# Kernel tuning notes

Hardware: AMD Instinct MI355X
Metric: run time of the kernel (lower is better)

Reference implementation:

```python
import jax, jax.numpy as jnp
import numpy as np

N_NODES = 50000
N_EDGES = 800000
OUT_DIM = 394
BN_EPS = 1e-5


def setup_inputs() -> dict:
    key = jax.random.key(0)
    ks = jax.random.split(key, 10)
    x = jax.random.normal(ks[0], (N_NODES, 2), dtype=jnp.float32)
    edge_index = jax.random.randint(ks[1], (2, N_EDGES), 0, N_NODES, dtype=jnp.int64)
    W_gcn = jax.random.normal(ks[2], (OUT_DIM, 2), dtype=jnp.float32) * 0.5
    b_gcn = jax.random.normal(ks[3], (OUT_DIM,), dtype=jnp.float32) * 0.1
    bn_gamma = jax.random.normal(ks[4], (OUT_DIM,), dtype=jnp.float32) * 0.1 + 1.0
    bn_beta = jax.random.normal(ks[5], (OUT_DIM,), dtype=jnp.float32) * 0.1
    bn_mean = jax.random.normal(ks[6], (OUT_DIM,), dtype=jnp.float32) * 0.1
    bn_var = jax.random.uniform(ks[7], (OUT_DIM,), dtype=jnp.float32, minval=0.5, maxval=1.5)
    fc_w = jax.random.normal(ks[8], (OUT_DIM, OUT_DIM), dtype=jnp.float32) * (1.0 / np.sqrt(OUT_DIM))
    fc_b = jax.random.normal(ks[9], (OUT_DIM,), dtype=jnp.float32) * 0.1
    return {"x": x, "edge_index": edge_index, "W_gcn": W_gcn, "b_gcn": b_gcn,
            "bn_gamma": bn_gamma, "bn_beta": bn_beta, "bn_mean": bn_mean,
            "bn_var": bn_var, "fc_w": fc_w, "fc_b": fc_b}


def reference(x, edge_index, W_gcn, b_gcn, bn_gamma, bn_beta, bn_mean, bn_var, fc_w, fc_b):
    n = x.shape[0]
    loop = jnp.arange(n, dtype=edge_index.dtype)
    # PyG GCNConv: add self-loops, symmetric deg^{-1/2} normalization
    src = jnp.concatenate([edge_index[0], loop])  # [E+N] message sources
    dst = jnp.concatenate([edge_index[1], loop])  # [E+N] message targets
    deg = jax.ops.segment_sum(jnp.ones_like(dst, dtype=x.dtype), dst, num_segments=n)
    dinv = jnp.where(deg > 0, jax.lax.rsqrt(deg), 0.0)
    norm = dinv[src] * dinv[dst]  # [E+N]
    xl = x @ W_gcn.T  # [N, 394] linear transform before aggregation
    msgs = xl[src] * norm[:, None]  # [E+N, 394] gathered + normalized messages
    agg = jax.ops.segment_sum(msgs, dst, num_segments=n) + b_gcn  # scatter-add
    h = jax.nn.relu(agg)
    # BatchNorm1d in eval mode (running stats)
    h = (h - bn_mean) * jax.lax.rsqrt(bn_var + BN_EPS) * bn_gamma + bn_beta
    # dropout is a no-op in eval mode
    z = h @ fc_w.T + fc_b
    return (jax.nn.log_softmax(z, axis=1), z)
```

## Files before the change

kernel.cpp:

```cpp
#include <hip/hip_runtime.h>
#include <math.h>

#define DIM 394
#define KP  416
#define NT  13
#define NP  448
#define BN_EPS 1e-5f
#define MAXD 32
#define TST 452

typedef __bf16 bf16x8 __attribute__((ext_vector_type(8)));
typedef float  f32x4  __attribute__((ext_vector_type(4)));

__device__ inline bool edges_are_int32(const int* ei) {
    int l = threadIdx.x & 63;
    unsigned long long b = __ballot(ei[2 * l + 1] != 0);
    return b != 0ULL;
}


__global__ void prep_kernel(const float* __restrict__ Wg, const float* __restrict__ bg,
                            const float* __restrict__ gamma, const float* __restrict__ beta,
                            const float* __restrict__ mean, const float* __restrict__ var,
                            const float* __restrict__ fcw,
                            uint4* __restrict__ zbase, float4* __restrict__ Pk,
                            float* __restrict__ Ok, bf16x8* __restrict__ Bp,
                            int z4, int zb) {
    int b = blockIdx.x, t = threadIdx.x;
    if (b < zb) {
        int i = b * 256 + t;
        if (i < z4) zbase[i] = make_uint4(0u, 0u, 0u, 0u);
    } else if (b < zb + 2) {
        int k = (b - zb) * 256 + t;
        if (k < KP) {
            float4 p = make_float4(0.f, 0.f, 0.f, 0.f);
            float o = 0.f;
            if (k < DIM) {
                p.x = Wg[2 * k];
                p.y = Wg[2 * k + 1];
                p.z = bg[k];
                float sc = gamma[k] * rsqrtf(var[k] + BN_EPS);
                p.w = sc;
                o = beta[k] - sc * mean[k];
            }
            Pk[k] = p;
            Ok[k] = o;
        }
    } else {
        int idx = (b - zb - 2) * 256 + t;
        if (idx < NT * 4 * NP) {
            int col = idx % NP;
            int r   = idx / NP;
            int k0  = r * 8;
            bf16x8 v;
            #pragma unroll
            for (int q = 0; q < 8; ++q) {
                int k = k0 + q;
                float f = (col < DIM && k < DIM) ? fcw[col * DIM + k] : 0.0f;
                v[q] = (__bf16)f;
            }
            Bp[idx] = v;
        }
    }
}

__global__ void place_kernel(const int* __restrict__ ei,
                             unsigned* __restrict__ degc,
                             unsigned* __restrict__ payload,
                             unsigned* __restrict__ ocnt,
                             uint2* __restrict__ olist, int e) {
    bool is32 = edges_are_int32(ei);
    int i0 = (blockIdx.x * blockDim.x + threadIdx.x) * 4;
    if (i0 >= e) return;
    int s[4], d[4];
    int cnt = 4;
    if (i0 + 4 <= e) {
        if (is32) {
            int4 sv = *reinterpret_cast<const int4*>(&ei[i0]);
            int4 dv = *reinterpret_cast<const int4*>(&ei[e + i0]);
            s[0] = sv.x; s[1] = sv.y; s[2] = sv.z; s[3] = sv.w;
            d[0] = dv.x; d[1] = dv.y; d[2] = dv.z; d[3] = dv.w;
        } else {
            int4 a = *reinterpret_cast<const int4*>(&ei[2 * i0]);
            int4 bb = *reinterpret_cast<const int4*>(&ei[2 * i0 + 4]);
            int4 c = *reinterpret_cast<const int4*>(&ei[2 * (e + i0)]);
            int4 dd = *reinterpret_cast<const int4*>(&ei[2 * (e + i0) + 4]);
            s[0] = a.x; s[1] = a.z; s[2] = bb.x; s[3] = bb.z;
            d[0] = c.x; d[1] = c.z; d[2] = dd.x; d[3] = dd.z;
        }
    } else {
        cnt = e - i0;
        for (int j = 0; j < cnt; ++j) {
            s[j] = is32 ? ei[i0 + j]     : ei[2 * (i0 + j)];
            d[j] = is32 ? ei[e + i0 + j] : ei[2 * (e + i0 + j)];
        }
    }
    #pragma unroll
    for (int j = 0; j < 4; ++j) {
        if (j >= cnt) break;
        unsigned tk = atomicAdd(&degc[d[j]], 1u);
        if (tk < MAXD) {
            payload[(size_t)d[j] * MAXD + tk] = (unsigned)s[j];
        } else {
            unsigned o = atomicAdd(ocnt, 1u);
            olist[o] = make_uint2((unsigned)s[j], (unsigned)d[j]);
        }
    }
}

__global__ void cleanup_kernel(const uint2* __restrict__ olist,
                               const unsigned* __restrict__ ocnt,
                               const unsigned* __restrict__ degc,
                               const float2* __restrict__ x2,
                               float* __restrict__ yover) {
    unsigned cnt = *ocnt;
    int gstride = gridDim.x * blockDim.x;
    for (unsigned i = blockIdx.x * blockDim.x + threadIdx.x; i < cnt; i += gstride) {
        uint2 sd = olist[i];
        float ds = rsqrtf(1.0f + (float)degc[sd.x]);
        float2 xv = x2[sd.x];
        atomicAdd(&yover[2 * sd.y],     ds * xv.x);
        atomicAdd(&yover[2 * sd.y + 1], ds * xv.y);
    }
}

__global__ __launch_bounds__(256, 2)
void gemm_fused(const float2* __restrict__ x2, const unsigned* __restrict__ degc,
                const unsigned* __restrict__ payload, const float* __restrict__ yover,
                const float4* __restrict__ Pk, const float* __restrict__ Ok,
                const bf16x8* __restrict__ Bp, const float* __restrict__ fcb,
                float* __restrict__ outp, float* __restrict__ z, int n) {
    __shared__ alignas(16) char smem[16 * TST * 4 + 64];
    bf16x8* As   = (bf16x8*)smem;
    float2* red  = (float2*)(smem + 8192);
    float*  T    = (float*)smem;
    float*  lsebuf = (float*)(smem + 16 * TST * 4);

    int tid = threadIdx.x;
    int wv  = tid >> 6;
    int l   = tid & 63;
    int cg_ = tid & 15;
    int kg  = l >> 4;
    int row0 = blockIdx.x * 64;
    int gi = row0 + l;

    float y0 = 0.f, y1 = 0.f;
    {
        float2 psum = make_float2(0.f, 0.f);
        float dinv_i = 0.f;
        float2 xi = make_float2(0.f, 0.f);
        if (gi < n) {
            unsigned dg = degc[gi];
            dinv_i = rsqrtf(1.0f + (float)dg);
            xi = x2[gi];
            unsigned m = dg < MAXD ? dg : MAXD;
            const unsigned* pl = payload + (size_t)gi * MAXD;
            for (unsigned t = wv; t < m; t += 4) {
                unsigned s = pl[t];
                float2 xv = x2[s];
                float ds = rsqrtf(1.0f + (float)degc[s]);
                psum.x = fmaf(ds, xv.x, psum.x);
                psum.y = fmaf(ds, xv.y, psum.y);
            }
            if (wv == 0) {
                psum.x += yover[2 * gi];
                psum.y += yover[2 * gi + 1];
            }
        }
        red[l * 4 + wv] = psum;
        __syncthreads();
        if (gi < n) {
            float sx = red[l * 4 + 0].x + red[l * 4 + 1].x + red[l * 4 + 2].x + red[l * 4 + 3].x;
            float sy = red[l * 4 + 0].y + red[l * 4 + 1].y + red[l * 4 + 2].y + red[l * 4 + 3].y;
            y0 = dinv_i * (sx + dinv_i * xi.x);
            y1 = dinv_i * (sy + dinv_i * xi.y);
        }
        __syncthreads();
    }

    f32x4 acc[4][7];
    #pragma unroll
    for (int a = 0; a < 4; ++a)
        #pragma unroll
        for (int b = 0; b < 7; ++b)
            acc[a][b] = (f32x4){0.f, 0.f, 0.f, 0.f};

    auto stageA = [&](int ks, int buf) {
        int kb = ks * 32 + wv * 8;
        bf16x8 hv;
        #pragma unroll
        for (int q = 0; q < 8; ++q) {
            float4 p = Pk[kb + q];
            float t = fmaf(y0, p.x, fmaf(y1, p.y, p.z));
            t = fmaxf(t, 0.f);
            hv[q] = (__bf16)fmaf(p.w, t, Ok[kb + q]);
        }
        As[buf * 256 + wv * 64 + l] = hv;
    };

    const bf16x8* bptr = Bp + (kg * 448 + wv * 112 + cg_);

    bf16x8 Bcur[7], Bnxt[7];
    #pragma unroll
    for (int c = 0; c < 7; ++c) Bcur[c] = bptr[c * 16];
    stageA(0, 0);
    __syncthreads();

    int buf = 0;
    for (int ks = 0; ks < NT; ++ks) {
        if (ks < NT - 1) {
            const bf16x8* bn = bptr + (size_t)(ks + 1) * (4 * 448);
            #pragma unroll
            for (int c = 0; c < 7; ++c) Bnxt[c] = bn[c * 16];
            stageA(ks + 1, buf ^ 1);
        }
        bf16x8 af[4];
        #pragma unroll
        for (int rt = 0; rt < 4; ++rt)
            af[rt] = As[buf * 256 + kg * 64 + rt * 16 + cg_];
        #pragma unroll
        for (int ct = 0; ct < 7; ++ct)
            #pragma unroll
            for (int rt = 0; rt < 4; ++rt)
                acc[rt][ct] = __builtin_amdgcn_mfma_f32_16x16x32_bf16(
                                  af[rt], Bcur[ct], acc[rt][ct], 0, 0, 0);
        __syncthreads();
        #pragma unroll
        for (int c = 0; c < 7; ++c) Bcur[c] = Bnxt[c];
        buf ^= 1;
    }

    float* redm = (float*)smem;
    float* reds = redm + 256;

    int colb = wv * 112;
    float bias[7];
    bool  cv[7];
    #pragma unroll
    for (int ct = 0; ct < 7; ++ct) {
        int c = colb + ct * 16 + cg_;
        cv[ct] = (c < DIM);
        bias[ct] = cv[ct] ? fcb[c] : 0.f;
    }
    #pragma unroll
    for (int rt = 0; rt < 4; ++rt)
        #pragma unroll
        for (int ct = 0; ct < 7; ++ct)
            acc[rt][ct] = acc[rt][ct] + bias[ct];

    f32x4 mx[4];
    #pragma unroll
    for (int rt = 0; rt < 4; ++rt) {
        f32x4 m = (f32x4){-1e30f, -1e30f, -1e30f, -1e30f};
        #pragma unroll
        for (int ct = 0; ct < 7; ++ct) {
            if (!cv[ct]) continue;
            #pragma unroll
            for (int j = 0; j < 4; ++j) m[j] = fmaxf(m[j], acc[rt][ct][j]);
        }
        #pragma unroll
        for (int msk = 1; msk < 16; msk <<= 1)
            #pragma unroll
            for (int j = 0; j < 4; ++j)
                m[j] = fmaxf(m[j], __shfl_xor(m[j], msk));
        mx[rt] = m;
    }
    if (cg_ == 0) {
        #pragma unroll
        for (int rt = 0; rt < 4; ++rt)
            #pragma unroll
            for (int j = 0; j < 4; ++j)
                redm[(rt * 16 + kg * 4 + j) * 4 + wv] = mx[rt][j];
    }
    __syncthreads();
    f32x4 gm[4];
    #pragma unroll
    for (int rt = 0; rt < 4; ++rt)
        #pragma unroll
        for (int j = 0; j < 4; ++j) {
            int r = (rt * 16 + kg * 4 + j) * 4;
            gm[rt][j] = fmaxf(fmaxf(redm[r], redm[r + 1]),
                              fmaxf(redm[r + 2], redm[r + 3]));
        }

    f32x4 sm[4];
    #pragma unroll
    for (int rt = 0; rt < 4; ++rt) {
        f32x4 s = (f32x4){0.f, 0.f, 0.f, 0.f};
        #pragma unroll
        for (int ct = 0; ct < 7; ++ct) {
            if (!cv[ct]) continue;
            #pragma unroll
            for (int j = 0; j < 4; ++j)
                s[j] += __expf(acc[rt][ct][j] - gm[rt][j]);
        }
        #pragma unroll
        for (int msk = 1; msk < 16; msk <<= 1)
            #pragma unroll
            for (int j = 0; j < 4; ++j)
                s[j] += __shfl_xor(s[j], msk);
        sm[rt] = s;
    }
    if (cg_ == 0) {
        #pragma unroll
        for (int rt = 0; rt < 4; ++rt)
            #pragma unroll
            for (int j = 0; j < 4; ++j)
                reds[(rt * 16 + kg * 4 + j) * 4 + wv] = sm[rt][j];
    }
    __syncthreads();
    f32x4 lse[4];
    #pragma unroll
    for (int rt = 0; rt < 4; ++rt)
        #pragma unroll
        for (int j = 0; j < 4; ++j) {
            int r = (rt * 16 + kg * 4 + j) * 4;
            float t = reds[r] + reds[r + 1] + reds[r + 2] + reds[r + 3];
            lse[rt][j] = gm[rt][j] + __logf(t);
        }
    __syncthreads();

    #pragma unroll
    for (int rt = 0; rt < 4; ++rt) {
        #pragma unroll
        for (int ct = 0; ct < 7; ++ct) {
            int c = colb + ct * 16 + cg_;
            #pragma unroll
            for (int j = 0; j < 4; ++j)
                T[(kg * 4 + j) * TST + c] = acc[rt][ct][j];
        }
        if (wv == 0 && cg_ == 0) {
            #pragma unroll
            for (int j = 0; j < 4; ++j)
                lsebuf[kg * 4 + j] = lse[rt][j];
        }
        __syncthreads();
        #pragma unroll
        for (int q = 0; q < 7; ++q) {
            int idx = tid + q * 256;
            int row = idx / 112;
            int c4  = idx - row * 112;
            int grow2 = row0 + rt * 16 + row;
            if (grow2 < n && c4 <= 98) {
                float4 v = *reinterpret_cast<const float4*>(&T[row * TST + c4 * 4]);
                float L = lsebuf[row];
                size_t base = (size_t)grow2 * DIM + c4 * 4;
                if (c4 <= 97) {
                    *reinterpret_cast<float2*>(&z[base])        = make_float2(v.x, v.y);
                    *reinterpret_cast<float2*>(&z[base + 2])    = make_float2(v.z, v.w);
                    *reinterpret_cast<float2*>(&outp[base])     = make_float2(v.x - L, v.y - L);
                    *reinterpret_cast<float2*>(&outp[base + 2]) = make_float2(v.z - L, v.w - L);
                } else {
                    *reinterpret_cast<float2*>(&z[base])    = make_float2(v.x, v.y);
                    *reinterpret_cast<float2*>(&outp[base]) = make_float2(v.x - L, v.y - L);
                }
            }
        }
        __syncthreads();
    }
}

extern "C" void kernel_launch(void* const* d_in, const int* in_sizes, int n_in,
                              void* d_out, int out_size, void* d_ws, size_t ws_size,
                              hipStream_t stream) {
    int n = in_sizes[0] / 2;
    int e = in_sizes[1] / 2;

    const float2* x2   = (const float2*)d_in[0];
    const int*   ei    = (const int*)d_in[1];
    const float* Wg    = (const float*)d_in[2];
    const float* bg    = (const float*)d_in[3];
    const float* gamma = (const float*)d_in[4];
    const float* beta  = (const float*)d_in[5];
    const float* mean  = (const float*)d_in[6];
    const float* var   = (const float*)d_in[7];
    const float* fcw   = (const float*)d_in[8];
    const float* fcb   = (const float*)d_in[9];

    float* out = (float*)d_out;
    float* z   = out + (size_t)n * DIM;

    char* wsb = (char*)d_ws;
    unsigned* degc  = (unsigned*)wsb;
    float*    yover = (float*)(degc + n);
    unsigned* ocnt  = (unsigned*)(yover + 2 * (size_t)n);
    uint2*    olist = (uint2*)(ocnt + 4);
    size_t off = (size_t)(3 * n + 4) * 4 + (size_t)e * 8;
    off = (off + 255) & ~(size_t)255;
    unsigned* payload = (unsigned*)(wsb + off);
    off += (size_t)n * MAXD * 4;
    off = (off + 255) & ~(size_t)255;
    bf16x8* Bp = (bf16x8*)(wsb + off);
    off += (size_t)NT * 4 * NP * 16;
    float4* Pk = (float4*)(wsb + off);
    off += (size_t)KP * 16;
    float* Ok  = (float*)(wsb + off);

    int zwords = 3 * n + 4;
    int z4 = (zwords + 3) / 4;
    int zb = (z4 + 255) / 256;
    int prep_blocks = zb + 2 + (NT * 4 * NP + 255) / 256;
    int eb4 = (e / 4 + 255) / 256 + 1;

    prep_kernel<<<prep_blocks, 256, 0, stream>>>(Wg, bg, gamma, beta, mean, var,
                                                 fcw, (uint4*)degc, Pk, Ok, Bp,
                                                 z4, zb);
    place_kernel<<<eb4, 256, 0, stream>>>(ei, degc, payload, ocnt, olist, e);
    cleanup_kernel<<<64, 256, 0, stream>>>(olist, ocnt, degc, x2, yover);

    int gm = (n + 63) / 64;
    gemm_fused<<<gm, 256, 0, stream>>>(x2, degc, payload, yover,
                                       Pk, Ok, Bp, fcb, out, z, n);
}
```

Measured before the change: 131.3 us.

## Precompute degree-scaled node features and stage BN/GCN params in LDS

A new pass computes xs = dinv*x per node once, merged into the overflow cleanup kernel. The aggregation loop in the fused GEMM then gathers one float2 per neighbor instead of a feature, a degree and an rsqrt. The per-column GCN and BN parameters are copied into shared memory so the A-staging loop reads LDS instead of global memory. The edge placement kernel now handles 8 edges per thread, and one barrier moves later in the kernel. The cost is an extra n-sized float2 buffer in the workspace. The cleanup loop now strides by 512 with two blocks, less parallelism for the overflow edges.

```diff
diff --git a/kernel.cpp b/kernel.cpp
--- a/kernel.cpp
+++ b/kernel.cpp
@@ -70,33 +70,43 @@
                              unsigned* __restrict__ ocnt,
                              uint2* __restrict__ olist, int e) {
     bool is32 = edges_are_int32(ei);
-    int i0 = (blockIdx.x * blockDim.x + threadIdx.x) * 4;
+    int i0 = (blockIdx.x * blockDim.x + threadIdx.x) * 8;
     if (i0 >= e) return;
-    int s[4], d[4];
-    int cnt = 4;
-    if (i0 + 4 <= e) {
+    int s[8], d[8];
+    int cnt = 8;
+    if (i0 + 8 <= e && (e & 7) == 0) {
         if (is32) {
-            int4 sv = *reinterpret_cast<const int4*>(&ei[i0]);
-            int4 dv = *reinterpret_cast<const int4*>(&ei[e + i0]);
-            s[0] = sv.x; s[1] = sv.y; s[2] = sv.z; s[3] = sv.w;
-            d[0] = dv.x; d[1] = dv.y; d[2] = dv.z; d[3] = dv.w;
+            int4 a0 = *reinterpret_cast<const int4*>(&ei[i0]);
+            int4 a1 = *reinterpret_cast<const int4*>(&ei[i0 + 4]);
+            int4 c0 = *reinterpret_cast<const int4*>(&ei[e + i0]);
+            int4 c1 = *reinterpret_cast<const int4*>(&ei[e + i0 + 4]);
+            s[0]=a0.x; s[1]=a0.y; s[2]=a0.z; s[3]=a0.w;
+            s[4]=a1.x; s[5]=a1.y; s[6]=a1.z; s[7]=a1.w;
+            d[0]=c0.x; d[1]=c0.y; d[2]=c0.z; d[3]=c0.w;
+            d[4]=c1.x; d[5]=c1.y; d[6]=c1.z; d[7]=c1.w;
         } else {
-            int4 a = *reinterpret_cast<const int4*>(&ei[2 * i0]);
-            int4 bb = *reinterpret_cast<const int4*>(&ei[2 * i0 + 4]);
-            int4 c = *reinterpret_cast<const int4*>(&ei[2 * (e + i0)]);
-            int4 dd = *reinterpret_cast<const int4*>(&ei[2 * (e + i0) + 4]);
-            s[0] = a.x; s[1] = a.z; s[2] = bb.x; s[3] = bb.z;
-            d[0] = c.x; d[1] = c.z; d[2] = dd.x; d[3] = dd.z;
+            int4 a0 = *reinterpret_cast<const int4*>(&ei[2 * i0]);
+            int4 a1 = *reinterpret_cast<const int4*>(&ei[2 * i0 + 4]);
+            int4 a2 = *reinterpret_cast<const int4*>(&ei[2 * i0 + 8]);
+            int4 a3 = *reinterpret_cast<const int4*>(&ei[2 * i0 + 12]);
+            int4 c0 = *reinterpret_cast<const int4*>(&ei[2 * (e + i0)]);
+            int4 c1 = *reinterpret_cast<const int4*>(&ei[2 * (e + i0) + 4]);
+            int4 c2 = *reinterpret_cast<const int4*>(&ei[2 * (e + i0) + 8]);
+            int4 c3 = *reinterpret_cast<const int4*>(&ei[2 * (e + i0) + 12]);
+            s[0]=a0.x; s[1]=a0.z; s[2]=a1.x; s[3]=a1.z;
+            s[4]=a2.x; s[5]=a2.z; s[6]=a3.x; s[7]=a3.z;
+            d[0]=c0.x; d[1]=c0.z; d[2]=c1.x; d[3]=c1.z;
+            d[4]=c2.x; d[5]=c2.z; d[6]=c3.x; d[7]=c3.z;
         }
     } else {
-        cnt = e - i0;
+        cnt = e - i0 < 8 ? e - i0 : 8;
         for (int j = 0; j < cnt; ++j) {
             s[j] = is32 ? ei[i0 + j]     : ei[2 * (i0 + j)];
             d[j] = is32 ? ei[e + i0 + j] : ei[2 * (e + i0 + j)];
         }
     }
     #pragma unroll
-    for (int j = 0; j < 4; ++j) {
+    for (int j = 0; j < 8; ++j) {
         if (j >= cnt) break;
         unsigned tk = atomicAdd(&degc[d[j]], 1u);
         if (tk < MAXD) {
@@ -108,31 +118,44 @@
     }
 }
 
-__global__ void cleanup_kernel(const uint2* __restrict__ olist,
-                               const unsigned* __restrict__ ocnt,
-                               const unsigned* __restrict__ degc,
-                               const float2* __restrict__ x2,
-                               float* __restrict__ yover) {
-    unsigned cnt = *ocnt;
-    int gstride = gridDim.x * blockDim.x;
-    for (unsigned i = blockIdx.x * blockDim.x + threadIdx.x; i < cnt; i += gstride) {
-        uint2 sd = olist[i];
-        float ds = rsqrtf(1.0f + (float)degc[sd.x]);
-        float2 xv = x2[sd.x];
-        atomicAdd(&yover[2 * sd.y],     ds * xv.x);
-        atomicAdd(&yover[2 * sd.y + 1], ds * xv.y);
+__global__ void xs_cleanup_kernel(const float2* __restrict__ x2,
+                                  const unsigned* __restrict__ degc,
+                                  float2* __restrict__ xs2,
+                                  const uint2* __restrict__ olist,
+                                  const unsigned* __restrict__ ocnt,
+                                  float* __restrict__ yover, int n, int nb0) {
+    int b = blockIdx.x;
+    if (b < nb0) {
+        int i = b * 256 + threadIdx.x;
+        if (i < n) {
+            float di = rsqrtf(1.0f + (float)degc[i]);
+            float2 xv = x2[i];
+            xs2[i] = make_float2(di * xv.x, di * xv.y);
+        }
+    } else {
+        unsigned cnt = *ocnt;
+        unsigned t = (b - nb0) * 256 + threadIdx.x;
+        for (unsigned i = t; i < cnt; i += 512) {
+            uint2 sd = olist[i];
+            float ds = rsqrtf(1.0f + (float)degc[sd.x]);
+            float2 xv = x2[sd.x];
+            atomicAdd(&yover[2 * sd.y],     ds * xv.x);
+            atomicAdd(&yover[2 * sd.y + 1], ds * xv.y);
+        }
     }
 }
 
 __global__ __launch_bounds__(256, 2)
-void gemm_fused(const float2* __restrict__ x2, const unsigned* __restrict__ degc,
+void gemm_fused(const float2* __restrict__ xs2, const unsigned* __restrict__ degc,
                 const unsigned* __restrict__ payload, const float* __restrict__ yover,
-                const float4* __restrict__ Pk, const float* __restrict__ Ok,
+                const float4* __restrict__ PkG, const float* __restrict__ OkG,
                 const bf16x8* __restrict__ Bp, const float* __restrict__ fcb,
                 float* __restrict__ outp, float* __restrict__ z, int n) {
     __shared__ alignas(16) char smem[16 * TST * 4 + 64];
     bf16x8* As   = (bf16x8*)smem;
     float2* red  = (float2*)(smem + 8192);
+    float4* PkL  = (float4*)(smem + 10240);
+    float*  OkL  = (float*)(smem + 16896);
     float*  T    = (float*)smem;
     float*  lsebuf = (float*)(smem + 16 * TST * 4);
 
@@ -144,23 +167,26 @@
     int row0 = blockIdx.x * 64;
     int gi = row0 + l;
 
+    for (int i = tid; i < KP; i += 256) {
+        PkL[i] = PkG[i];
+        OkL[i] = OkG[i];
+    }
+
     float y0 = 0.f, y1 = 0.f;
     {
         float2 psum = make_float2(0.f, 0.f);
         float dinv_i = 0.f;
-        float2 xi = make_float2(0.f, 0.f);
+        float2 xsg = make_float2(0.f, 0.f);
         if (gi < n) {
             unsigned dg = degc[gi];
             dinv_i = rsqrtf(1.0f + (float)dg);
-            xi = x2[gi];
+            xsg = xs2[gi];
             unsigned m = dg < MAXD ? dg : MAXD;
             const unsigned* pl = payload + (size_t)gi * MAXD;
             for (unsigned t = wv; t < m; t += 4) {
-                unsigned s = pl[t];
-                float2 xv = x2[s];
-                float ds = rsqrtf(1.0f + (float)degc[s]);
-                psum.x = fmaf(ds, xv.x, psum.x);
-                psum.y = fmaf(ds, xv.y, psum.y);
+                float2 xv = xs2[pl[t]];
+                psum.x += xv.x;
+                psum.y += xv.y;
             }
             if (wv == 0) {
                 psum.x += yover[2 * gi];
@@ -172,10 +198,9 @@
         if (gi < n) {
             float sx = red[l * 4 + 0].x + red[l * 4 + 1].x + red[l * 4 + 2].x + red[l * 4 + 3].x;
             float sy = red[l * 4 + 0].y + red[l * 4 + 1].y + red[l * 4 + 2].y + red[l * 4 + 3].y;
-            y0 = dinv_i * (sx + dinv_i * xi.x);
-            y1 = dinv_i * (sy + dinv_i * xi.y);
-        }
-        __syncthreads();
+            y0 = dinv_i * (sx + xsg.x);
+            y1 = dinv_i * (sy + xsg.y);
+        }
     }
 
     f32x4 acc[4][7];
@@ -190,10 +215,10 @@
         bf16x8 hv;
         #pragma unroll
         for (int q = 0; q < 8; ++q) {
-            float4 p = Pk[kb + q];
+            float4 p = PkL[kb + q];
             float t = fmaf(y0, p.x, fmaf(y1, p.y, p.z));
             t = fmaxf(t, 0.f);
-            hv[q] = (__bf16)fmaf(p.w, t, Ok[kb + q]);
+            hv[q] = (__bf16)fmaf(p.w, t, OkL[kb + q]);
         }
         As[buf * 256 + wv * 64 + l] = hv;
     };
@@ -265,6 +290,7 @@
                 m[j] = fmaxf(m[j], __shfl_xor(m[j], msk));
         mx[rt] = m;
     }
+    __syncthreads();
     if (cg_ == 0) {
         #pragma unroll
         for (int rt = 0; rt < 4; ++rt)
@@ -384,8 +410,9 @@
     unsigned* degc  = (unsigned*)wsb;
     float*    yover = (float*)(degc + n);
     unsigned* ocnt  = (unsigned*)(yover + 2 * (size_t)n);
-    uint2*    olist = (uint2*)(ocnt + 4);
-    size_t off = (size_t)(3 * n + 4) * 4 + (size_t)e * 8;
+    float2*   xs2   = (float2*)(ocnt + 4);
+    uint2*    olist = (uint2*)(xs2 + n);
+    size_t off = (size_t)(5 * n + 4) * 4 + (size_t)e * 8;
     off = (off + 255) & ~(size_t)255;
     unsigned* payload = (unsigned*)(wsb + off);
     off += (size_t)n * MAXD * 4;
@@ -400,15 +427,17 @@
     int z4 = (zwords + 3) / 4;
     int zb = (z4 + 255) / 256;
     int prep_blocks = zb + 2 + (NT * 4 * NP + 255) / 256;
-    int eb4 = (e / 4 + 255) / 256 + 1;
+    int eb8 = (e / 8 + 255) / 256 + 1;
+    int nb0 = (n + 255) / 256;
 
     prep_kernel<<<prep_blocks, 256, 0, stream>>>(Wg, bg, gamma, beta, mean, var,
                                                  fcw, (uint4*)degc, Pk, Ok, Bp,
                                                  z4, zb);
-    place_kernel<<<eb4, 256, 0, stream>>>(ei, degc, payload, ocnt, olist, e);
-    cleanup_kernel<<<64, 256, 0, stream>>>(olist, ocnt, degc, x2, yover);
+    place_kernel<<<eb8, 256, 0, stream>>>(ei, degc, payload, ocnt, olist, e);
+    xs_cleanup_kernel<<<nb0 + 2, 256, 0, stream>>>(x2, degc, xs2, olist, ocnt,
+                                                   yover, n, nb0);
 
     int gm = (n + 63) / 64;
-    gemm_fused<<<gm, 256, 0, stream>>>(x2, degc, payload, yover,
+    gemm_fused<<<gm, 256, 0, stream>>>(xs2, degc, payload, yover,
                                        Pk, Ok, Bp, fcb, out, z, n);
 }
```

Measured after the change: 123.0 us. 6.4% less time.
